# Kernel tuning notes

Measured on AMD Instinct MI355X. Metric: run time of the kernel, lower is better.

## Reference

```python
import math
import jax, jax.numpy as jnp
import numpy as np

B, H, S, D = 2, 16, 2048, 64
NEG = -1000000000.0


def setup_inputs() -> dict:
    key = jax.random.key(0)
    kq, kk, kv = jax.random.split(key, 3)
    q = jax.random.normal(kq, (B, H, S, D), dtype=jnp.float32)
    k = jax.random.normal(kk, (B, H, S, D), dtype=jnp.float32)
    v = jax.random.normal(kv, (B, H, S, D), dtype=jnp.float32)
    attention_mask = jnp.ones((B, S), dtype=jnp.float32)
    return {"q": q, "k": k, "v": v, "attention_mask": attention_mask}


def reference(q, k, v, attention_mask):
    head_dim = q.shape[-1]
    scaling = 1.0 / math.sqrt(head_dim)
    # scores: [B, H, S, S]
    scores = jnp.einsum("bhqd,bhkd->bhqk", q, k) * scaling
    seq_len = q.shape[-2]
    # causal mask: upper triangle (excluding diag) gets large negative
    causal_mask = jnp.triu(jnp.full((seq_len, seq_len), NEG, dtype=scores.dtype), k=1)
    scores = scores + causal_mask[None, None, :, :]
    # additive attention mask: [B,1,1,S]
    add_mask = (1.0 - attention_mask)[:, None, None, :] * NEG
    scores = scores + add_mask
    weights = jax.nn.softmax(scores, axis=-1)  # dropout p=0.0 -> identity
    out = jnp.einsum("bhqk,bhkd->bhqd", weights, v)
    return out
```

## Files before the change

kernel.cpp:

```cpp
#include <hip/hip_runtime.h>

typedef _Float16 half8 __attribute__((ext_vector_type(8)));
typedef _Float16 half4 __attribute__((ext_vector_type(4)));
typedef float f32x4 __attribute__((ext_vector_type(4)));

#define MFMA_F16 __builtin_amdgcn_mfma_f32_16x16x32_f16

constexpr int Bc = 2, Hc = 16, Sc = 2048, Dc = 64;
constexpr int QBLK = 64, KVBLK = 64;
constexpr int NQT = Sc / QBLK;
constexpr float LOG2E = 1.4426950408889634f;
constexpr float SCALE_LOG2E = 0.125f * LOG2E;
constexpr float NEGBIG = -1.0e9f;
constexpr int LDK = 72;


__global__ __launch_bounds__(256, 4)
void sdpa_p1(const float* __restrict__ Q, const float* __restrict__ K,
             const float* __restrict__ V, const float* __restrict__ AM,
             float* __restrict__ Oacc, float* __restrict__ Lsum)
{
    __shared__ _Float16 Kh[2][KVBLK][LDK];
    __shared__ _Float16 Vt[2][Dc][LDK];
    __shared__ float    madd[2][KVBLK];

    const int bid = blockIdx.x;
    const int xcd = bid & 7;
    const int lid = bid >> 3;
    const int bh  = xcd + 8 * (lid / 48);
    const int j   = lid % 48;
    int qt, kv0, kv1;
    if (j < 32) {
        qt = 31 - (j >> 1);
        const int h = (qt + 2) >> 1;
        kv0 = (j & 1) ? h : 0;
        kv1 = (j & 1) ? (qt + 1) : h;
    } else {
        qt = 47 - j;
        kv0 = 0; kv1 = qt + 1;
    }
    const int b  = bh >> 4;
    const int qb = qt * QBLK;

    const int t    = threadIdx.x;
    const int w    = t >> 6;
    const int lane = t & 63;
    const int l16  = lane & 15;
    const int hi   = lane >> 4;
    const int hi4  = hi * 4;

    const size_t base = (size_t)bh * Sc * Dc;

    const int srow = t >> 4;
    const int sd0  = (t & 15) * 4;
    const int ssw  = (t & 7) << 3;

    float4 kreg[4], vreg[4];
    float  amreg = 0.f;

    auto stage_load = [&](int kvt_) {
        const int kvb = kvt_ * KVBLK;
        #pragma unroll
        for (int i = 0; i < 4; ++i) {
            const size_t g = base + (size_t)(kvb + srow + 16 * i) * Dc + sd0;
            kreg[i] = *(const float4*)(K + g);
            vreg[i] = *(const float4*)(V + g);
        }
        if (t < KVBLK) amreg = AM[(size_t)b * Sc + kvb + t];
    };
    auto stage_write = [&](int bf) {
        #pragma unroll
        for (int i = 0; i < 4; ++i) {
            const int kv = srow + 16 * i;
            half4 kh = { (_Float16)kreg[i].x, (_Float16)kreg[i].y,
                         (_Float16)kreg[i].z, (_Float16)kreg[i].w };
            *(half4*)(&Kh[bf][kv][sd0]) = kh;
            const int pos = ((kv >> 5) << 5) | (((kv >> 2) & 3) << 3)
                          | (((kv >> 4) & 1) << 2) | (kv & 3);
            const int col = pos ^ ssw;
            Vt[bf][sd0 + 0][col] = (_Float16)vreg[i].x;
            Vt[bf][sd0 + 1][col] = (_Float16)vreg[i].y;
            Vt[bf][sd0 + 2][col] = (_Float16)vreg[i].z;
            Vt[bf][sd0 + 3][col] = (_Float16)vreg[i].w;
        }
        if (t < KVBLK) madd[bf][t] = (1.0f - amreg) * (NEGBIG * LOG2E);
    };

    half8 qfrag[2];
    {
        const float* qp = Q + base + (size_t)(qb + w * 16 + l16) * Dc + hi * 8;
        #pragma unroll
        for (int c = 0; c < 2; ++c) {
            float4 x0 = *(const float4*)(qp + c * 32);
            float4 x1 = *(const float4*)(qp + c * 32 + 4);
            qfrag[c] = (half8){
                (_Float16)(x0.x * SCALE_LOG2E), (_Float16)(x0.y * SCALE_LOG2E),
                (_Float16)(x0.z * SCALE_LOG2E), (_Float16)(x0.w * SCALE_LOG2E),
                (_Float16)(x1.x * SCALE_LOG2E), (_Float16)(x1.y * SCALE_LOG2E),
                (_Float16)(x1.z * SCALE_LOG2E), (_Float16)(x1.w * SCALE_LOG2E) };
        }
    }

    f32x4 o[4];
    #pragma unroll
    for (int dt = 0; dt < 4; ++dt) o[dt] = (f32x4){0.f, 0.f, 0.f, 0.f};
    float lacc = 0.f;

    stage_load(kv0);
    stage_write(0);
    __syncthreads();

    const int qg = qb + w * 16 + l16;

    for (int kvt = kv0; kvt < kv1; ++kvt) {
        const int cur  = (kvt - kv0) & 1;
        const bool pref = (kvt + 1 < kv1);
        if (pref) stage_load(kvt + 1);

        f32x4 st[4];
        #pragma unroll
        for (int nt = 0; nt < 4; ++nt) {
            st[nt] = (f32x4){0.f, 0.f, 0.f, 0.f};
            #pragma unroll
            for (int c = 0; c < 2; ++c) {
                half8 kf = *(const half8*)(&Kh[cur][nt * 16 + l16][c * 32 + hi * 8]);
                st[nt] = MFMA_F16(kf, qfrag[c], st[nt], 0, 0, 0);
            }
        }

        #pragma unroll
        for (int nt = 0; nt < 4; ++nt) {
            const f32x4 mr = *(const f32x4*)(&madd[cur][nt * 16 + hi4]);
            #pragma unroll
            for (int r = 0; r < 4; ++r) st[nt][r] += mr[r];
        }
        if (kvt == qt) {
            const int kvb = kvt * KVBLK;
            #pragma unroll
            for (int nt = 0; nt < 4; ++nt)
                #pragma unroll
                for (int r = 0; r < 4; ++r)
                    if (kvb + nt * 16 + hi4 + r > qg) st[nt][r] = NEGBIG;
        }

        #pragma unroll
        for (int nt = 0; nt < 4; ++nt)
            #pragma unroll
            for (int r = 0; r < 4; ++r) {
                const float p = exp2f(st[nt][r]);
                lacc += p;
                st[nt][r] = p;
            }

        half8 pa[2];
        #pragma unroll
        for (int c = 0; c < 2; ++c)
            #pragma unroll
            for (int jj = 0; jj < 8; ++jj)
                pa[c][jj] = (_Float16)st[2 * c + (jj >> 2)][jj & 3];

        #pragma unroll
        for (int dt = 0; dt < 4; ++dt) {
            const int row = dt * 16 + l16;
            const int sw  = ((row >> 2) & 7) << 3;
            const half8 vf0 = *(const half8*)(&Vt[cur][row][(hi * 8) ^ sw]);
            const half8 vf1 = *(const half8*)(&Vt[cur][row][(32 + hi * 8) ^ sw]);
            o[dt] = MFMA_F16(pa[0], vf0, o[dt], 0, 0, 0);
            o[dt] = MFMA_F16(pa[1], vf1, o[dt], 0, 0, 0);
        }

        if (pref) {
            stage_write(cur ^ 1);
            __syncthreads();
        }
    }

    lacc += __shfl_xor(lacc, 16);
    lacc += __shfl_xor(lacc, 32);
    if (hi == 0)
        unsafeAtomicAdd(&Lsum[(size_t)bh * Sc + qb + w * 16 + l16], lacc);

    float* op = Oacc + base + (size_t)(qb + w * 16 + hi4) * Dc + l16;
    #pragma unroll
    for (int r = 0; r < 4; ++r)
        #pragma unroll
        for (int dt = 0; dt < 4; ++dt)
            unsafeAtomicAdd(&op[(size_t)r * Dc + dt * 16], o[dt][r]);
}

__global__ __launch_bounds__(256)
void sdpa_norm(float* __restrict__ O, const float* __restrict__ L)
{
    const int i = blockIdx.x * 256 + threadIdx.x;
    float4* o4 = (float4*)O;
    float4 v = o4[i];
    const float inv = 1.0f / L[i >> 4];
    v.x *= inv; v.y *= inv; v.z *= inv; v.w *= inv;
    o4[i] = v;
}

__global__ __launch_bounds__(256)
void sdpa_zero(float4* __restrict__ O4, float4* __restrict__ L4)
{
    const int i = blockIdx.x * 256 + threadIdx.x;
    const float4 z = {0.f, 0.f, 0.f, 0.f};
    O4[i] = z;
    O4[i + 524288] = z;
    if (i < 16384) L4[i] = z;
}

extern "C" void kernel_launch(void* const* d_in, const int* in_sizes, int n_in,
                              void* d_out, int out_size, void* d_ws, size_t ws_size,
                              hipStream_t stream)
{
    const float* q  = (const float*)d_in[0];
    const float* k  = (const float*)d_in[1];
    const float* v  = (const float*)d_in[2];
    const float* am = (const float*)d_in[3];
    float* out = (float*)d_out;
    float* L   = (float*)d_ws;

    sdpa_zero<<<2048, 256, 0, stream>>>((float4*)out, (float4*)L);
    sdpa_p1<<<1536, 256, 0, stream>>>(q, k, v, am, out, L);
    sdpa_norm<<<4096, 256, 0, stream>>>(out, L);
}
```

Before: 146.4 us.

## Split causal KV range into more chunks, single-buffer LDS, raise occupancy

```diff
diff --git a/kernel.cpp b/kernel.cpp
--- a/kernel.cpp
+++ b/kernel.cpp
@@ -15,30 +15,30 @@
 constexpr int LDK = 72;
 
 
-__global__ __launch_bounds__(256, 4)
+__global__ __launch_bounds__(256, 8)
 void sdpa_p1(const float* __restrict__ Q, const float* __restrict__ K,
              const float* __restrict__ V, const float* __restrict__ AM,
              float* __restrict__ Oacc, float* __restrict__ Lsum)
 {
-    __shared__ _Float16 Kh[2][KVBLK][LDK];
-    __shared__ _Float16 Vt[2][Dc][LDK];
-    __shared__ float    madd[2][KVBLK];
+    __shared__ _Float16 Kh[KVBLK][LDK];
+    __shared__ _Float16 Vt[Dc][LDK];
+    __shared__ float    madd[KVBLK];
 
     const int bid = blockIdx.x;
-    const int xcd = bid & 7;
-    const int lid = bid >> 3;
-    const int bh  = xcd + 8 * (lid / 48);
-    const int j   = lid % 48;
-    int qt, kv0, kv1;
-    if (j < 32) {
-        qt = 31 - (j >> 1);
-        const int h = (qt + 2) >> 1;
-        kv0 = (j & 1) ? h : 0;
-        kv1 = (j & 1) ? (qt + 1) : h;
-    } else {
-        qt = 47 - j;
-        kv0 = 0; kv1 = qt + 1;
-    }
+    const int bh  = bid & 31;
+    const int c0  = (bid >> 5) & 7;
+    const int kk  = bid >> 8;
+    const int j   = ((kk & 1) ? (7 - c0) : c0) + 8 * kk;
+
+    int qt, c, nc;
+    if (j < 8)       { qt = j;                 c = 0;            nc = 1; }
+    else if (j < 24) { qt = 8 + ((j - 8) >> 1);  c = (j - 8) & 1;  nc = 2; }
+    else if (j < 48) { qt = 16 + (j - 24) / 3;   c = (j - 24) % 3; nc = 3; }
+    else             { qt = 24 + ((j - 48) >> 2); c = (j - 48) & 3; nc = 4; }
+    const int n   = qt + 1;
+    const int kv0 = c * n / nc;
+    const int kv1 = (c + 1) * n / nc;
+
     const int b  = bh >> 4;
     const int qb = qt * QBLK;
 
@@ -68,32 +68,32 @@
         }
         if (t < KVBLK) amreg = AM[(size_t)b * Sc + kvb + t];
     };
-    auto stage_write = [&](int bf) {
+    auto stage_write = [&]() {
         #pragma unroll
         for (int i = 0; i < 4; ++i) {
             const int kv = srow + 16 * i;
             half4 kh = { (_Float16)kreg[i].x, (_Float16)kreg[i].y,
                          (_Float16)kreg[i].z, (_Float16)kreg[i].w };
-            *(half4*)(&Kh[bf][kv][sd0]) = kh;
+            *(half4*)(&Kh[kv][sd0]) = kh;
             const int pos = ((kv >> 5) << 5) | (((kv >> 2) & 3) << 3)
                           | (((kv >> 4) & 1) << 2) | (kv & 3);
             const int col = pos ^ ssw;
-            Vt[bf][sd0 + 0][col] = (_Float16)vreg[i].x;
-            Vt[bf][sd0 + 1][col] = (_Float16)vreg[i].y;
-            Vt[bf][sd0 + 2][col] = (_Float16)vreg[i].z;
-            Vt[bf][sd0 + 3][col] = (_Float16)vreg[i].w;
-        }
-        if (t < KVBLK) madd[bf][t] = (1.0f - amreg) * (NEGBIG * LOG2E);
+            Vt[sd0 + 0][col] = (_Float16)vreg[i].x;
+            Vt[sd0 + 1][col] = (_Float16)vreg[i].y;
+            Vt[sd0 + 2][col] = (_Float16)vreg[i].z;
+            Vt[sd0 + 3][col] = (_Float16)vreg[i].w;
+        }
+        if (t < KVBLK) madd[t] = (1.0f - amreg) * (NEGBIG * LOG2E);
     };
 
     half8 qfrag[2];
     {
         const float* qp = Q + base + (size_t)(qb + w * 16 + l16) * Dc + hi * 8;
         #pragma unroll
-        for (int c = 0; c < 2; ++c) {
-            float4 x0 = *(const float4*)(qp + c * 32);
-            float4 x1 = *(const float4*)(qp + c * 32 + 4);
-            qfrag[c] = (half8){
+        for (int cc = 0; cc < 2; ++cc) {
+            float4 x0 = *(const float4*)(qp + cc * 32);
+            float4 x1 = *(const float4*)(qp + cc * 32 + 4);
+            qfrag[cc] = (half8){
                 (_Float16)(x0.x * SCALE_LOG2E), (_Float16)(x0.y * SCALE_LOG2E),
                 (_Float16)(x0.z * SCALE_LOG2E), (_Float16)(x0.w * SCALE_LOG2E),
                 (_Float16)(x1.x * SCALE_LOG2E), (_Float16)(x1.y * SCALE_LOG2E),
@@ -107,13 +107,12 @@
     float lacc = 0.f;
 
     stage_load(kv0);
-    stage_write(0);
+    stage_write();
     __syncthreads();
 
     const int qg = qb + w * 16 + l16;
 
     for (int kvt = kv0; kvt < kv1; ++kvt) {
-        const int cur  = (kvt - kv0) & 1;
         const bool pref = (kvt + 1 < kv1);
         if (pref) stage_load(kvt + 1);
 
@@ -122,15 +121,15 @@
         for (int nt = 0; nt < 4; ++nt) {
             st[nt] = (f32x4){0.f, 0.f, 0.f, 0.f};
             #pragma unroll
-            for (int c = 0; c < 2; ++c) {
-                half8 kf = *(const half8*)(&Kh[cur][nt * 16 + l16][c * 32 + hi * 8]);
-                st[nt] = MFMA_F16(kf, qfrag[c], st[nt], 0, 0, 0);
+            for (int cc = 0; cc < 2; ++cc) {
+                half8 kf = *(const half8*)(&Kh[nt * 16 + l16][cc * 32 + hi * 8]);
+                st[nt] = MFMA_F16(kf, qfrag[cc], st[nt], 0, 0, 0);
             }
         }
 
         #pragma unroll
         for (int nt = 0; nt < 4; ++nt) {
-            const f32x4 mr = *(const f32x4*)(&madd[cur][nt * 16 + hi4]);
+            const f32x4 mr = *(const f32x4*)(&madd[nt * 16 + hi4]);
             #pragma unroll
             for (int r = 0; r < 4; ++r) st[nt][r] += mr[r];
         }
@@ -154,23 +153,24 @@
 
         half8 pa[2];
         #pragma unroll
-        for (int c = 0; c < 2; ++c)
+        for (int cc = 0; cc < 2; ++cc)
             #pragma unroll
             for (int jj = 0; jj < 8; ++jj)
-                pa[c][jj] = (_Float16)st[2 * c + (jj >> 2)][jj & 3];
+                pa[cc][jj] = (_Float16)st[2 * cc + (jj >> 2)][jj & 3];
 
         #pragma unroll
         for (int dt = 0; dt < 4; ++dt) {
             const int row = dt * 16 + l16;
             const int sw  = ((row >> 2) & 7) << 3;
-            const half8 vf0 = *(const half8*)(&Vt[cur][row][(hi * 8) ^ sw]);
-            const half8 vf1 = *(const half8*)(&Vt[cur][row][(32 + hi * 8) ^ sw]);
+            const half8 vf0 = *(const half8*)(&Vt[row][(hi * 8) ^ sw]);
+            const half8 vf1 = *(const half8*)(&Vt[row][(32 + hi * 8) ^ sw]);
             o[dt] = MFMA_F16(pa[0], vf0, o[dt], 0, 0, 0);
             o[dt] = MFMA_F16(pa[1], vf1, o[dt], 0, 0, 0);
         }
 
         if (pref) {
-            stage_write(cur ^ 1);
+            __syncthreads();
+            stage_write();
             __syncthreads();
         }
     }
@@ -221,6 +221,6 @@
     float* L   = (float*)d_ws;
 
     sdpa_zero<<<2048, 256, 0, stream>>>((float4*)out, (float4*)L);
-    sdpa_p1<<<1536, 256, 0, stream>>>(q, k, v, am, out, L);
+    sdpa_p1<<<2560, 256, 0, stream>>>(q, k, v, am, out, L);
     sdpa_norm<<<4096, 256, 0, stream>>>(out, L);
 }
```

Result: slower. 354.3 us (+142.0%).
